# Performance work log

Hardware: AMD Instinct MI355X
Metric: run time of the kernel (lower is better)

The kernel has to match this reference:

```python
import jax, jax.numpy as jnp
import numpy as np

EMBED = 1024
HEADS = 16
HEAD_SIZE = EMBED // HEADS


def setup_inputs() -> dict:
    key = jax.random.key(0)
    kx, kk, kq, kv, kp, kb = jax.random.split(key, 6)
    s = 1.0 / np.sqrt(EMBED)
    return {
        "x": jax.random.normal(kx, (4, 2048, EMBED), dtype=jnp.float32),
        "Wk": jax.random.uniform(kk, (EMBED, EMBED), jnp.float32, -s, s),
        "Wq": jax.random.uniform(kq, (EMBED, EMBED), jnp.float32, -s, s),
        "Wv": jax.random.uniform(kv, (EMBED, EMBED), jnp.float32, -s, s),
        "Wp": jax.random.uniform(kp, (EMBED, EMBED), jnp.float32, -s, s),
        "bp": jax.random.uniform(kb, (EMBED,), jnp.float32, -s, s),
    }


def reference(x, Wk, Wq, Wv, Wp, bp):
    B, T, C = x.shape
    H, D = HEADS, HEAD_SIZE
    # torch nn.Linear: y = x @ W.T
    k = (x @ Wk.T).reshape(B, T, H, D).transpose(0, 2, 1, 3)  # [B,H,T,D]
    q = (x @ Wq.T).reshape(B, T, H, D).transpose(0, 2, 1, 3)
    v = (x @ Wv.T).reshape(B, T, H, D).transpose(0, 2, 1, 3)
    att = jnp.einsum('bhqd,bhkd->bhqk', q, k) * (1.0 / np.sqrt(D))
    causal = jnp.tril(jnp.ones((T, T), dtype=bool))
    att = jnp.where(causal, att, -jnp.inf)
    att = jax.nn.softmax(att, axis=-1)
    # dropout is identity in eval mode
    out = jnp.einsum('bhqk,bhkd->bhqd', att, v)
    out = out.transpose(0, 2, 1, 3).reshape(B, T, C)
    return out @ Wp.T + bp
```

## Files before the change

kernel.cpp:

```cpp
#include <hip/hip_runtime.h>
#include <hip/hip_bf16.h>

typedef __attribute__((ext_vector_type(8))) short bf16x8;
typedef __attribute__((ext_vector_type(4))) float f32x4;

#define DEVINL __device__ __forceinline__

static DEVINL ushort f2b(float f) {
    union { float f; unsigned int u; } v; v.f = f;
    unsigned int u = v.u;
    unsigned int r = (u + 0x7FFFu + ((u >> 16) & 1u)) >> 16;
    return (ushort)r;
}

static DEVINL unsigned int cvtpk(float lo, float hi) {
    unsigned int r;
    asm("v_cvt_pk_bf16_f32 %0, %1, %2" : "=v"(r) : "v"(lo), "v"(hi));
    return r;
}

static DEVINL void gload_lds16(const ushort* g, ushort* l) {
    __builtin_amdgcn_global_load_lds(
        (const __attribute__((address_space(1))) unsigned int*)g,
        (__attribute__((address_space(3))) unsigned int*)l,
        16, 0, 0);
}

static DEVINL int swz(int row, int c) {
    return row * 64 + (((c ^ (row & 7)) & 7) << 3);
}

__global__ void cast_w_kernel(const float* __restrict__ Wq, const float* __restrict__ Wk,
                              const float* __restrict__ Wv, const float* __restrict__ Wp,
                              ushort* __restrict__ out) {
    int idx = blockIdx.x * blockDim.x + threadIdx.x;
    int col4 = idx & 255;
    int row  = idx >> 8;
    int which = row >> 10;
    int r = row & 1023;
    const float* src = (which == 0) ? Wq : (which == 1) ? Wk : (which == 2) ? Wv : Wp;
    float s = (which == 0) ? 0.125f : 1.0f;
    float4 v = ((const float4*)src)[r * 256 + col4];
    ushort4 o;
    o.x = f2b(v.x * s); o.y = f2b(v.y * s); o.z = f2b(v.z * s); o.w = f2b(v.w * s);
    ((ushort4*)out)[idx] = o;
}

__global__ void cast_x_kernel(const float* __restrict__ x, ushort* __restrict__ out) {
    int idx = blockIdx.x * blockDim.x + threadIdx.x;
    float4 v = ((const float4*)x)[idx];
    ushort4 o;
    o.x = f2b(v.x); o.y = f2b(v.y); o.z = f2b(v.z); o.w = f2b(v.w);
    ((ushort4*)out)[idx] = o;
}

template<bool BF16_OUT>
__global__ __launch_bounds__(256) void gemm_bt_kernel(const ushort* __restrict__ A,
                                                      const ushort* __restrict__ B,
                                                      void* __restrict__ Cv,
                                                      const float* __restrict__ bias,
                                                      int M, int N, int K, int gx) {
    __shared__ ushort Al[128 * 64];
    __shared__ ushort Bl[128 * 64];
    const int tid = threadIdx.x;

    const int nwg = (int)gridDim.x;
    const int cpx = nwg >> 3;
    const int orig = (int)blockIdx.x;
    const int wgid = (orig & 7) * cpx + (orig >> 3);
    const int bx = wgid % gx, by = wgid / gx;
    const int m0 = by * 128, n0 = bx * 128;

    const int lane = tid & 63, wid = tid >> 6;
    const int wm = (wid >> 1) * 64, wn = (wid & 1) * 64;
    const int lr = lane & 15, lg = lane >> 4;

    f32x4 acc[4][4];
    #pragma unroll
    for (int i = 0; i < 4; ++i)
        #pragma unroll
        for (int j = 0; j < 4; ++j)
            acc[i][j] = (f32x4){0.f, 0.f, 0.f, 0.f};

    const int grow = wid * 32 + (lane >> 3);
    const int gcol = (((lane & 7) ^ (lane >> 3)) & 7) * 8;
    const ushort* ga = A + (size_t)(m0 + grow) * K + gcol;
    const ushort* gb = B + (size_t)(n0 + grow) * K + gcol;
    ushort* la = &Al[wid * 32 * 64];
    ushort* lb = &Bl[wid * 32 * 64];

    const int nkt = K >> 6;
    for (int kt = 0; kt < nkt; ++kt) {
        const int kof = kt * 64;
        __syncthreads();
        #pragma unroll
        for (int j = 0; j < 4; ++j) {
            gload_lds16(ga + (size_t)(j * 8) * K + kof, la + j * 8 * 64);
            gload_lds16(gb + (size_t)(j * 8) * K + kof, lb + j * 8 * 64);
        }
        __syncthreads();
        #pragma unroll
        for (int kk = 0; kk < 64; kk += 32) {
            bf16x8 af[4], bfr[4];
            #pragma unroll
            for (int mi = 0; mi < 4; ++mi)
                af[mi] = *(const bf16x8*)&Al[swz(wm + mi * 16 + lr, (kk >> 3) + lg)];
            #pragma unroll
            for (int ni = 0; ni < 4; ++ni)
                bfr[ni] = *(const bf16x8*)&Bl[swz(wn + ni * 16 + lr, (kk >> 3) + lg)];
            #pragma unroll
            for (int mi = 0; mi < 4; ++mi)
                #pragma unroll
                for (int ni = 0; ni < 4; ++ni)
                    acc[mi][ni] = __builtin_amdgcn_mfma_f32_16x16x32_bf16(af[mi], bfr[ni], acc[mi][ni], 0, 0, 0);
        }
    }
    #pragma unroll
    for (int mi = 0; mi < 4; ++mi) {
        #pragma unroll
        for (int r = 0; r < 4; ++r) {
            int gm = m0 + wm + mi * 16 + lg * 4 + r;
            #pragma unroll
            for (int ni = 0; ni < 4; ++ni) {
                int gn = n0 + wn + ni * 16 + lr;
                float val = acc[mi][ni][r];
                if (BF16_OUT) {
                    ((ushort*)Cv)[(size_t)gm * N + gn] = f2b(val);
                } else {
                    ((float*)Cv)[(size_t)gm * N + gn] = val + bias[gn];
                }
            }
        }
    }
}

__global__ void transpose_v_kernel(const ushort* __restrict__ QKV, ushort* __restrict__ Vt) {
    __shared__ ushort tile[32][33];
    int t0 = blockIdx.x * 32;
    int n0 = blockIdx.y * 32;
    int tx = threadIdx.x, ty = threadIdx.y;
    #pragma unroll
    for (int i = 0; i < 4; ++i) {
        int row = ty + i * 8;
        tile[row][tx] = QKV[(size_t)(t0 + row) * 3072 + 2048 + n0 + tx];
    }
    __syncthreads();
    #pragma unroll
    for (int i = 0; i < 4; ++i) {
        int row = ty + i * 8;
        Vt[(size_t)(n0 + row) * 8192 + t0 + tx] = tile[tx][row];
    }
}

__global__ __launch_bounds__(256, 3) void attn_kernel(const ushort* __restrict__ QKV,
                                                      const ushort* __restrict__ Vt,
                                                      ushort* __restrict__ O) {
    __shared__ ushort Kl[2][64 * 64];
    __shared__ ushort Vl[2][64 * 64];
    __shared__ ushort Pl[4][32 * 64];

    const int bh = blockIdx.x, b = bh >> 4, h = bh & 15;
    const int qb = (int)gridDim.y - 1 - (int)blockIdx.y;
    const int q0 = qb * 128;
    const int tid = threadIdx.x, lane = tid & 63, w = tid >> 6;
    const int lr = lane & 15, lg = lane >> 4;
    const int qw = q0 + w * 32;

    bf16x8 qf[2][2];
    {
        const ushort* qp = QKV + (size_t)(b * 2048 + qw + lr) * 3072 + h * 64 + lg * 8;
        qf[0][0] = *(const bf16x8*)qp;
        qf[0][1] = *(const bf16x8*)(qp + 32);
        qf[1][0] = *(const bf16x8*)(qp + (size_t)16 * 3072);
        qf[1][1] = *(const bf16x8*)(qp + (size_t)16 * 3072 + 32);
    }

    f32x4 o[4][2];
    #pragma unroll
    for (int di = 0; di < 4; ++di)
        #pragma unroll
        for (int nt_ = 0; nt_ < 2; ++nt_)
            o[di][nt_] = (f32x4){0.f, 0.f, 0.f, 0.f};
    float mrow[2] = {-INFINITY, -INFINITY};
    float lrow[2] = {0.f, 0.f};

    const size_t kbase = (size_t)(b * 2048) * 3072 + 1024 + h * 64;
    const size_t vbase = (size_t)(h * 64) * 8192 + (size_t)b * 2048;
    const int srow = tid >> 2, sc = tid & 3;
    const int ss0 = swz(srow, sc), ss1 = swz(srow, sc + 4);
    char* const pw = (char*)&Pl[w][0];

    const int nt = qb * 2 + 2;
    uint4 kr0, kr1, vr0, vr1;

    #define LOADT(t) do {                                                      \
        const int kv0s = (t) * 64;                                             \
        const ushort* kg = QKV + kbase + (size_t)(kv0s + srow) * 3072;         \
        const ushort* vg = Vt + vbase + (size_t)srow * 8192 + kv0s;            \
        kr0 = *(const uint4*)&kg[sc * 8];                                      \
        kr1 = *(const uint4*)&kg[sc * 8 + 32];                                 \
        vr0 = *(const uint4*)&vg[sc * 8];                                      \
        vr1 = *(const uint4*)&vg[sc * 8 + 32];                                 \
    } while (0)

    #define WRITET(bufi) do {                                                  \
        *(uint4*)&Kl[bufi][ss0] = kr0;                                         \
        *(uint4*)&Kl[bufi][ss1] = kr1;                                         \
        *(uint4*)&Vl[bufi][ss0] = vr0;                                         \
        *(uint4*)&Vl[bufi][ss1] = vr1;                                         \
    } while (0)

    LOADT(0);
    WRITET(0);
    __syncthreads();

    for (int t = 0; t < nt; ++t) {
        const int buf = t & 1;
        const int kv0 = t * 64;
        const bool have_next = (t + 1 < nt);
        if (have_next) LOADT(t + 1);

        if (kv0 <= qw + 31) {
            f32x4 s[4][2];
            #pragma unroll
            for (int mi = 0; mi < 4; ++mi)
                #pragma unroll
                for (int nt_ = 0; nt_ < 2; ++nt_)
                    s[mi][nt_] = (f32x4){0.f, 0.f, 0.f, 0.f};
            __builtin_amdgcn_s_setprio(1);
            #pragma unroll
            for (int ks = 0; ks < 2; ++ks) {
                #pragma unroll
                for (int mi = 0; mi < 4; ++mi) {
                    bf16x8 kf = *(const bf16x8*)&Kl[buf][swz(mi * 16 + lr, ks * 4 + lg)];
                    s[mi][0] = __builtin_amdgcn_mfma_f32_16x16x32_bf16(kf, qf[0][ks], s[mi][0], 0, 0, 0);
                    s[mi][1] = __builtin_amdgcn_mfma_f32_16x16x32_bf16(kf, qf[1][ks], s[mi][1], 0, 0, 0);
                }
            }
            __builtin_amdgcn_s_setprio(0);

            #pragma unroll
            for (int nt_ = 0; nt_ < 2; ++nt_) {
                const int qn = qw + nt_ * 16 + lr;
                const bool full = (kv0 + 63 <= qw + nt_ * 16);
                const int kvb = kv0 + lg * 4;
                float v[4][4];
                #pragma unroll
                for (int mi = 0; mi < 4; ++mi)
                    #pragma unroll
                    for (int r = 0; r < 4; ++r) {
                        float x = s[mi][nt_][r];
                        if (!full) x = (kvb + mi * 16 + r <= qn) ? x : -INFINITY;
                        v[mi][r] = x;
                    }
                float mx0 = fmaxf(fmaxf(v[0][0], v[0][1]), fmaxf(v[0][2], v[0][3]));
                float mx1 = fmaxf(fmaxf(v[1][0], v[1][1]), fmaxf(v[1][2], v[1][3]));
                float mx2 = fmaxf(fmaxf(v[2][0], v[2][1]), fmaxf(v[2][2], v[2][3]));
                float mx3 = fmaxf(fmaxf(v[3][0], v[3][1]), fmaxf(v[3][2], v[3][3]));
                float pmax = fmaxf(fmaxf(mx0, mx1), fmaxf(mx2, mx3));
                pmax = fmaxf(pmax, __shfl_xor(pmax, 16));
                pmax = fmaxf(pmax, __shfl_xor(pmax, 32));

                const bool defer = __all(pmax <= mrow[nt_] + 8.0f);
                float mn;
                if (defer) {
                    mn = mrow[nt_];
                } else {
                    mn = fmaxf(mrow[nt_], pmax);
                    const float al = __expf(mrow[nt_] - mn);
                    lrow[nt_] *= al;
                    #pragma unroll
                    for (int di = 0; di < 4; ++di)
                        #pragma unroll
                        for (int r = 0; r < 4; ++r)
                            o[di][nt_][r] *= al;
                    mrow[nt_] = mn;
                }
                float p[4][4];
                #pragma unroll
                for (int mi = 0; mi < 4; ++mi)
                    #pragma unroll
                    for (int r = 0; r < 4; ++r)
                        p[mi][r] = __expf(v[mi][r] - mn);
                float rs = ((p[0][0] + p[0][1]) + (p[0][2] + p[0][3]))
                         + ((p[1][0] + p[1][1]) + (p[1][2] + p[1][3]))
                         + ((p[2][0] + p[2][1]) + (p[2][2] + p[2][3]))
                         + ((p[3][0] + p[3][1]) + (p[3][2] + p[3][3]));
                rs += __shfl_xor(rs, 16);
                rs += __shfl_xor(rs, 32);
                lrow[nt_] += rs;

                const int rowoff = (nt_ * 16 + lr) * 128;
                const int xr = (lr & 7) << 4;
                #pragma unroll
                for (int mi = 0; mi < 4; ++mi) {
                    uint2 val;
                    val.x = cvtpk(p[mi][0], p[mi][1]);
                    val.y = cvtpk(p[mi][2], p[mi][3]);
                    *(uint2*)(pw + rowoff + ((32 * mi + 8 * lg) ^ xr)) = val;
                }
            }
            asm volatile("s_waitcnt lgkmcnt(0)" ::: "memory");
            __builtin_amdgcn_sched_barrier(0);

            __builtin_amdgcn_s_setprio(1);
            #pragma unroll
            for (int ks = 0; ks < 2; ++ks) {
                bf16x8 pb[2];
                #pragma unroll
                for (int nt_ = 0; nt_ < 2; ++nt_) {
                    const int byteoff = (nt_ * 16 + lr) * 128 + (((64 * ks + 16 * lg)) ^ ((lr & 7) << 4));
                    pb[nt_] = *(const bf16x8*)(pw + byteoff);
                }
                #pragma unroll
                for (int di = 0; di < 4; ++di) {
                    bf16x8 vf = *(const bf16x8*)&Vl[buf][swz(di * 16 + lr, ks * 4 + lg)];
                    o[di][0] = __builtin_amdgcn_mfma_f32_16x16x32_bf16(vf, pb[0], o[di][0], 0, 0, 0);
                    o[di][1] = __builtin_amdgcn_mfma_f32_16x16x32_bf16(vf, pb[1], o[di][1], 0, 0, 0);
                }
            }
            __builtin_amdgcn_s_setprio(0);
        }
        if (have_next) WRITET(buf ^ 1);
        __syncthreads();
    }
    #undef LOADT
    #undef WRITET

    #pragma unroll
    for (int nt_ = 0; nt_ < 2; ++nt_) {
        const float inv = 1.0f / lrow[nt_];
        const int rowoff = (nt_ * 16 + lr) * 128;
        const int xr = (lr & 7) << 4;
        #pragma unroll
        for (int di = 0; di < 4; ++di) {
            uint2 val;
            val.x = cvtpk(o[di][nt_][0] * inv, o[di][nt_][1] * inv);
            val.y = cvtpk(o[di][nt_][2] * inv, o[di][nt_][3] * inv);
            *(uint2*)(pw + rowoff + ((32 * di + 8 * lg) ^ xr)) = val;
        }
    }
    asm volatile("s_waitcnt lgkmcnt(0)" ::: "memory");
    __builtin_amdgcn_sched_barrier(0);
    {
        const int row = lane >> 1;
        const int half = lane & 1;
        const int xr2 = (row & 7) << 4;
        ushort* og = O + (size_t)(b * 2048 + qw + row) * 1024 + h * 64 + half * 32;
        #pragma unroll
        for (int c = 0; c < 4; ++c) {
            uint4 val = *(const uint4*)(pw + row * 128 + ((half * 64 + c * 16) ^ xr2));
            *(uint4*)&og[c * 8] = val;
        }
    }
}

extern "C" void kernel_launch(void* const* d_in, const int* in_sizes, int n_in,
                              void* d_out, int out_size, void* d_ws, size_t ws_size,
                              hipStream_t stream) {
    const float* x  = (const float*)d_in[0];
    const float* Wk = (const float*)d_in[1];
    const float* Wq = (const float*)d_in[2];
    const float* Wv = (const float*)d_in[3];
    const float* Wp = (const float*)d_in[4];
    const float* bp = (const float*)d_in[5];
    float* out = (float*)d_out;

    char* ws = (char*)d_ws;
    ushort* Xb   = (ushort*)(ws);
    ushort* Wcat = (ushort*)(ws + 16777216);
    ushort* QKV  = (ushort*)(ws + 25165824);
    ushort* Vt   = (ushort*)(ws + 75497472);
    ushort* Obuf = (ushort*)(ws + 92274688);

    cast_w_kernel<<<4096, 256, 0, stream>>>(Wq, Wk, Wv, Wp, Wcat);
    cast_x_kernel<<<8192, 256, 0, stream>>>(x, Xb);
    gemm_bt_kernel<true><<<1536, 256, 0, stream>>>(Xb, Wcat, QKV, nullptr, 8192, 3072, 1024, 24);
    transpose_v_kernel<<<dim3(256, 32), dim3(32, 8), 0, stream>>>(QKV, Vt);
    attn_kernel<<<dim3(64, 16), 256, 0, stream>>>(QKV, Vt, Obuf);
    gemm_bt_kernel<false><<<512, 256, 0, stream>>>(Obuf, Wcat + (size_t)3072 * 1024, out, bp, 8192, 1024, 1024, 8);
}
```

Measured before the change: 185.1 us.

## Single-buffer attention K/V LDS, raise occupancy, use exp2 softmax, remap blocks

Folds log2(e) into the Q weight scale so the softmax can use exp2f instead of __expf, and widens the deferred-rescale threshold to match base-2 units. Drops the double-buffered K/V shared tiles to a single buffer with an extra barrier before the write, which cuts LDS per block so launch bounds can request 5 blocks per CU. The grid is flattened to 1D with a custom block-to-(batch, head, q-block) mapping that interleaves heads and keeps heavy causal blocks scheduled first. Risks: the extra sync serializes the LDS write with compute, and the higher occupancy target may force register spills.

```diff
diff --git a/kernel.cpp b/kernel.cpp
--- a/kernel.cpp
+++ b/kernel.cpp
@@ -39,7 +39,7 @@
     int which = row >> 10;
     int r = row & 1023;
     const float* src = (which == 0) ? Wq : (which == 1) ? Wk : (which == 2) ? Wv : Wp;
-    float s = (which == 0) ? 0.125f : 1.0f;
+    float s = (which == 0) ? 0.180336880111f : 1.0f;
     float4 v = ((const float4*)src)[r * 256 + col4];
     ushort4 o;
     o.x = f2b(v.x * s); o.y = f2b(v.y * s); o.z = f2b(v.z * s); o.w = f2b(v.w * s);
@@ -152,15 +152,17 @@
     }
 }
 
-__global__ __launch_bounds__(256, 3) void attn_kernel(const ushort* __restrict__ QKV,
+__global__ __launch_bounds__(256, 5) void attn_kernel(const ushort* __restrict__ QKV,
                                                       const ushort* __restrict__ Vt,
                                                       ushort* __restrict__ O) {
-    __shared__ ushort Kl[2][64 * 64];
-    __shared__ ushort Vl[2][64 * 64];
+    __shared__ ushort Kl[64 * 64];
+    __shared__ ushort Vl[64 * 64];
     __shared__ ushort Pl[4][32 * 64];
 
-    const int bh = blockIdx.x, b = bh >> 4, h = bh & 15;
-    const int qb = (int)gridDim.y - 1 - (int)blockIdx.y;
+    const int flat = (int)blockIdx.x;
+    const int bh = (flat & 7) * 8 + ((flat >> 7) & 7);
+    const int qb = 15 - ((flat >> 3) & 15);
+    const int b = bh >> 4, h = bh & 15;
     const int q0 = qb * 128;
     const int tid = threadIdx.x, lane = tid & 63, w = tid >> 6;
     const int lr = lane & 15, lg = lane >> 4;
@@ -203,19 +205,18 @@
         vr1 = *(const uint4*)&vg[sc * 8 + 32];                                 \
     } while (0)
 
-    #define WRITET(bufi) do {                                                  \
-        *(uint4*)&Kl[bufi][ss0] = kr0;                                         \
-        *(uint4*)&Kl[bufi][ss1] = kr1;                                         \
-        *(uint4*)&Vl[bufi][ss0] = vr0;                                         \
-        *(uint4*)&Vl[bufi][ss1] = vr1;                                         \
+    #define WRITET() do {                                                      \
+        *(uint4*)&Kl[ss0] = kr0;                                               \
+        *(uint4*)&Kl[ss1] = kr1;                                               \
+        *(uint4*)&Vl[ss0] = vr0;                                               \
+        *(uint4*)&Vl[ss1] = vr1;                                               \
     } while (0)
 
     LOADT(0);
-    WRITET(0);
+    WRITET();
     __syncthreads();
 
     for (int t = 0; t < nt; ++t) {
-        const int buf = t & 1;
         const int kv0 = t * 64;
         const bool have_next = (t + 1 < nt);
         if (have_next) LOADT(t + 1);
@@ -232,7 +233,7 @@
             for (int ks = 0; ks < 2; ++ks) {
                 #pragma unroll
                 for (int mi = 0; mi < 4; ++mi) {
-                    bf16x8 kf = *(const bf16x8*)&Kl[buf][swz(mi * 16 + lr, ks * 4 + lg)];
+                    bf16x8 kf = *(const bf16x8*)&Kl[swz(mi * 16 + lr, ks * 4 + lg)];
                     s[mi][0] = __builtin_amdgcn_mfma_f32_16x16x32_bf16(kf, qf[0][ks], s[mi][0], 0, 0, 0);
                     s[mi][1] = __builtin_amdgcn_mfma_f32_16x16x32_bf16(kf, qf[1][ks], s[mi][1], 0, 0, 0);
                 }
@@ -261,13 +262,13 @@
                 pmax = fmaxf(pmax, __shfl_xor(pmax, 16));
                 pmax = fmaxf(pmax, __shfl_xor(pmax, 32));
 
-                const bool defer = __all(pmax <= mrow[nt_] + 8.0f);
+                const bool defer = __all(pmax <= mrow[nt_] + 11.5f);
                 float mn;
                 if (defer) {
                     mn = mrow[nt_];
                 } else {
                     mn = fmaxf(mrow[nt_], pmax);
-                    const float al = __expf(mrow[nt_] - mn);
+                    const float al = exp2f(mrow[nt_] - mn);
                     lrow[nt_] *= al;
                     #pragma unroll
                     for (int di = 0; di < 4; ++di)
@@ -281,7 +282,7 @@
                 for (int mi = 0; mi < 4; ++mi)
                     #pragma unroll
                     for (int r = 0; r < 4; ++r)
-                        p[mi][r] = __expf(v[mi][r] - mn);
+                        p[mi][r] = exp2f(v[mi][r] - mn);
                 float rs = ((p[0][0] + p[0][1]) + (p[0][2] + p[0][3]))
                          + ((p[1][0] + p[1][1]) + (p[1][2] + p[1][3]))
                          + ((p[2][0] + p[2][1]) + (p[2][2] + p[2][3]))
@@ -314,14 +315,15 @@
                 }
                 #pragma unroll
                 for (int di = 0; di < 4; ++di) {
-                    bf16x8 vf = *(const bf16x8*)&Vl[buf][swz(di * 16 + lr, ks * 4 + lg)];
+                    bf16x8 vf = *(const bf16x8*)&Vl[swz(di * 16 + lr, ks * 4 + lg)];
                     o[di][0] = __builtin_amdgcn_mfma_f32_16x16x32_bf16(vf, pb[0], o[di][0], 0, 0, 0);
                     o[di][1] = __builtin_amdgcn_mfma_f32_16x16x32_bf16(vf, pb[1], o[di][1], 0, 0, 0);
                 }
             }
             __builtin_amdgcn_s_setprio(0);
         }
-        if (have_next) WRITET(buf ^ 1);
+        __syncthreads();
+        if (have_next) WRITET();
         __syncthreads();
     }
     #undef LOADT
@@ -377,6 +379,6 @@
     cast_x_kernel<<<8192, 256, 0, stream>>>(x, Xb);
     gemm_bt_kernel<true><<<1536, 256, 0, stream>>>(Xb, Wcat, QKV, nullptr, 8192, 3072, 1024, 24);
     transpose_v_kernel<<<dim3(256, 32), dim3(32, 8), 0, stream>>>(QKV, Vt);
-    attn_kernel<<<dim3(64, 16), 256, 0, stream>>>(QKV, Vt, Obuf);
+    attn_kernel<<<1024, 256, 0, stream>>>(QKV, Vt, Obuf);
     gemm_bt_kernel<false><<<512, 256, 0, stream>>>(Obuf, Wcat + (size_t)3072 * 1024, out, bp, 8192, 1024, 1024, 8);
 }
```

New measurement: 484.1 us. 162% more time.

## Fold log2e into Q scale, use exp2, and halve per-wave P staging LDS

Applied to the files above, without the earlier changes.

The Q weight scale now folds in log2(e), so the softmax uses exp2f directly instead of __expf. This removes a multiply per exponential, and the lazy-rescale threshold is converted to log2 units to match. The per-wave P staging buffer is halved: P is written and read back one k-slice at a time, and the output epilogue is done in two 16-row halves. This cuts LDS use per block, which may allow higher occupancy, at the cost of extra LDS waits and sched barriers inside the PV loop.

```diff
diff --git a/kernel.cpp b/kernel.cpp
--- a/kernel.cpp
+++ b/kernel.cpp
@@ -39,7 +39,7 @@
     int which = row >> 10;
     int r = row & 1023;
     const float* src = (which == 0) ? Wq : (which == 1) ? Wk : (which == 2) ? Wv : Wp;
-    float s = (which == 0) ? 0.125f : 1.0f;
+    float s = (which == 0) ? 0.180336880111f : 1.0f;
     float4 v = ((const float4*)src)[r * 256 + col4];
     ushort4 o;
     o.x = f2b(v.x * s); o.y = f2b(v.y * s); o.z = f2b(v.z * s); o.w = f2b(v.w * s);
@@ -157,7 +157,7 @@
                                                       ushort* __restrict__ O) {
     __shared__ ushort Kl[2][64 * 64];
     __shared__ ushort Vl[2][64 * 64];
-    __shared__ ushort Pl[4][32 * 64];
+    __shared__ ushort Pl[4][32 * 32];
 
     const int bh = blockIdx.x, b = bh >> 4, h = bh & 15;
     const int qb = (int)gridDim.y - 1 - (int)blockIdx.y;
@@ -189,6 +189,7 @@
     const int srow = tid >> 2, sc = tid & 3;
     const int ss0 = swz(srow, sc), ss1 = swz(srow, sc + 4);
     char* const pw = (char*)&Pl[w][0];
+    const int psx = ((lr >> 1) & 3) << 4;
 
     const int nt = qb * 2 + 2;
     uint4 kr0, kr1, vr0, vr1;
@@ -239,6 +240,7 @@
             }
             __builtin_amdgcn_s_setprio(0);
 
+            unsigned int px[2][4], py[2][4];
             #pragma unroll
             for (int nt_ = 0; nt_ < 2; ++nt_) {
                 const int qn = qw + nt_ * 16 + lr;
@@ -261,13 +263,13 @@
                 pmax = fmaxf(pmax, __shfl_xor(pmax, 16));
                 pmax = fmaxf(pmax, __shfl_xor(pmax, 32));
 
-                const bool defer = __all(pmax <= mrow[nt_] + 8.0f);
+                const bool defer = __all(pmax <= mrow[nt_] + 11.5f);
                 float mn;
                 if (defer) {
                     mn = mrow[nt_];
                 } else {
                     mn = fmaxf(mrow[nt_], pmax);
-                    const float al = __expf(mrow[nt_] - mn);
+                    const float al = exp2f(mrow[nt_] - mn);
                     lrow[nt_] *= al;
                     #pragma unroll
                     for (int di = 0; di < 4; ++di)
@@ -281,7 +283,7 @@
                 for (int mi = 0; mi < 4; ++mi)
                     #pragma unroll
                     for (int r = 0; r < 4; ++r)
-                        p[mi][r] = __expf(v[mi][r] - mn);
+                        p[mi][r] = exp2f(v[mi][r] - mn);
                 float rs = ((p[0][0] + p[0][1]) + (p[0][2] + p[0][3]))
                          + ((p[1][0] + p[1][1]) + (p[1][2] + p[1][3]))
                          + ((p[2][0] + p[2][1]) + (p[2][2] + p[2][3]))
@@ -290,36 +292,42 @@
                 rs += __shfl_xor(rs, 32);
                 lrow[nt_] += rs;
 
-                const int rowoff = (nt_ * 16 + lr) * 128;
-                const int xr = (lr & 7) << 4;
                 #pragma unroll
                 for (int mi = 0; mi < 4; ++mi) {
-                    uint2 val;
-                    val.x = cvtpk(p[mi][0], p[mi][1]);
-                    val.y = cvtpk(p[mi][2], p[mi][3]);
-                    *(uint2*)(pw + rowoff + ((32 * mi + 8 * lg) ^ xr)) = val;
+                    px[nt_][mi] = cvtpk(p[mi][0], p[mi][1]);
+                    py[nt_][mi] = cvtpk(p[mi][2], p[mi][3]);
                 }
             }
-            asm volatile("s_waitcnt lgkmcnt(0)" ::: "memory");
-            __builtin_amdgcn_sched_barrier(0);
-
-            __builtin_amdgcn_s_setprio(1);
+
             #pragma unroll
             for (int ks = 0; ks < 2; ++ks) {
+                #pragma unroll
+                for (int nt_ = 0; nt_ < 2; ++nt_) {
+                    const int rb = (nt_ * 16 + lr) * 64;
+                    #pragma unroll
+                    for (int m1 = 0; m1 < 2; ++m1) {
+                        const int mi = 2 * ks + m1;
+                        uint2 val;
+                        val.x = px[nt_][mi];
+                        val.y = py[nt_][mi];
+                        *(uint2*)(pw + rb + ((m1 * 32 + lg * 8) ^ psx)) = val;
+                    }
+                }
+                asm volatile("s_waitcnt lgkmcnt(0)" ::: "memory");
+                __builtin_amdgcn_sched_barrier(0);
+                __builtin_amdgcn_s_setprio(1);
                 bf16x8 pb[2];
                 #pragma unroll
-                for (int nt_ = 0; nt_ < 2; ++nt_) {
-                    const int byteoff = (nt_ * 16 + lr) * 128 + (((64 * ks + 16 * lg)) ^ ((lr & 7) << 4));
-                    pb[nt_] = *(const bf16x8*)(pw + byteoff);
-                }
+                for (int nt_ = 0; nt_ < 2; ++nt_)
+                    pb[nt_] = *(const bf16x8*)(pw + (nt_ * 16 + lr) * 64 + ((lg * 16) ^ psx));
                 #pragma unroll
                 for (int di = 0; di < 4; ++di) {
                     bf16x8 vf = *(const bf16x8*)&Vl[buf][swz(di * 16 + lr, ks * 4 + lg)];
                     o[di][0] = __builtin_amdgcn_mfma_f32_16x16x32_bf16(vf, pb[0], o[di][0], 0, 0, 0);
                     o[di][1] = __builtin_amdgcn_mfma_f32_16x16x32_bf16(vf, pb[1], o[di][1], 0, 0, 0);
                 }
+                __builtin_amdgcn_s_setprio(0);
             }
-            __builtin_amdgcn_s_setprio(0);
         }
         if (have_next) WRITET(buf ^ 1);
         __syncthreads();
@@ -330,27 +338,22 @@
     #pragma unroll
     for (int nt_ = 0; nt_ < 2; ++nt_) {
         const float inv = 1.0f / lrow[nt_];
-        const int rowoff = (nt_ * 16 + lr) * 128;
-        const int xr = (lr & 7) << 4;
         #pragma unroll
         for (int di = 0; di < 4; ++di) {
             uint2 val;
             val.x = cvtpk(o[di][nt_][0] * inv, o[di][nt_][1] * inv);
             val.y = cvtpk(o[di][nt_][2] * inv, o[di][nt_][3] * inv);
-            *(uint2*)(pw + rowoff + ((32 * di + 8 * lg) ^ xr)) = val;
-        }
-    }
-    asm volatile("s_waitcnt lgkmcnt(0)" ::: "memory");
-    __builtin_amdgcn_sched_barrier(0);
-    {
-        const int row = lane >> 1;
-        const int half = lane & 1;
-        const int xr2 = (row & 7) << 4;
-        ushort* og = O + (size_t)(b * 2048 + qw + row) * 1024 + h * 64 + half * 32;
-        #pragma unroll
-        for (int c = 0; c < 4; ++c) {
-            uint4 val = *(const uint4*)(pw + row * 128 + ((half * 64 + c * 16) ^ xr2));
-            *(uint4*)&og[c * 8] = val;
+            *(uint2*)(pw + lr * 128 + di * 32 + lg * 8) = val;
+        }
+        asm volatile("s_waitcnt lgkmcnt(0)" ::: "memory");
+        __builtin_amdgcn_sched_barrier(0);
+        {
+            const int row = lane >> 2, c = lane & 3;
+            ushort* og = O + (size_t)(b * 2048 + qw + nt_ * 16 + row) * 1024 + h * 64 + c * 16;
+            uint4 v0 = *(const uint4*)(pw + row * 128 + c * 32);
+            uint4 v1 = *(const uint4*)(pw + row * 128 + c * 32 + 16);
+            *(uint4*)og = v0;
+            *(uint4*)(og + 8) = v1;
         }
     }
 }
```

Result: slower. 196.3 us (+6.0%).

## Feed softmax probabilities to PV MFMA from registers, use exp2 with folded scale

Applied to the files above, without the earlier changes.

The probability tile no longer round-trips through a per-wave LDS buffer. P values stay in registers as packed bf16 and feed 16x16x16 MFMAs directly, with the V fragment loads reshaped to match that register layout. This removes LDS stores, the wait and the reloads, and frees the Pl shared array, which could raise occupancy; the epilogue reuses Kl as scratch. The Q scale now folds in log2(e) so exp2f replaces __expf, and the deferred-rescale threshold is raised to match base 2. The trade is twice as many, smaller MFMA instructions for the PV product.

```diff
diff --git a/kernel.cpp b/kernel.cpp
--- a/kernel.cpp
+++ b/kernel.cpp
@@ -2,6 +2,7 @@
 #include <hip/hip_bf16.h>
 
 typedef __attribute__((ext_vector_type(8))) short bf16x8;
+typedef __attribute__((ext_vector_type(4))) short bf16x4;
 typedef __attribute__((ext_vector_type(4))) float f32x4;
 
 #define DEVINL __device__ __forceinline__
@@ -39,7 +40,7 @@
     int which = row >> 10;
     int r = row & 1023;
     const float* src = (which == 0) ? Wq : (which == 1) ? Wk : (which == 2) ? Wv : Wp;
-    float s = (which == 0) ? 0.125f : 1.0f;
+    float s = (which == 0) ? 0.180336880111f : 1.0f;
     float4 v = ((const float4*)src)[r * 256 + col4];
     ushort4 o;
     o.x = f2b(v.x * s); o.y = f2b(v.y * s); o.z = f2b(v.z * s); o.w = f2b(v.w * s);
@@ -157,7 +158,6 @@
                                                       ushort* __restrict__ O) {
     __shared__ ushort Kl[2][64 * 64];
     __shared__ ushort Vl[2][64 * 64];
-    __shared__ ushort Pl[4][32 * 64];
 
     const int bh = blockIdx.x, b = bh >> 4, h = bh & 15;
     const int qb = (int)gridDim.y - 1 - (int)blockIdx.y;
@@ -188,7 +188,6 @@
     const size_t vbase = (size_t)(h * 64) * 8192 + (size_t)b * 2048;
     const int srow = tid >> 2, sc = tid & 3;
     const int ss0 = swz(srow, sc), ss1 = swz(srow, sc + 4);
-    char* const pw = (char*)&Pl[w][0];
 
     const int nt = qb * 2 + 2;
     uint4 kr0, kr1, vr0, vr1;
@@ -239,6 +238,7 @@
             }
             __builtin_amdgcn_s_setprio(0);
 
+            unsigned int px[2][4], py[2][4];
             #pragma unroll
             for (int nt_ = 0; nt_ < 2; ++nt_) {
                 const int qn = qw + nt_ * 16 + lr;
@@ -261,13 +261,13 @@
                 pmax = fmaxf(pmax, __shfl_xor(pmax, 16));
                 pmax = fmaxf(pmax, __shfl_xor(pmax, 32));
 
-                const bool defer = __all(pmax <= mrow[nt_] + 8.0f);
+                const bool defer = __all(pmax <= mrow[nt_] + 11.5f);
                 float mn;
                 if (defer) {
                     mn = mrow[nt_];
                 } else {
                     mn = fmaxf(mrow[nt_], pmax);
-                    const float al = __expf(mrow[nt_] - mn);
+                    const float al = exp2f(mrow[nt_] - mn);
                     lrow[nt_] *= al;
                     #pragma unroll
                     for (int di = 0; di < 4; ++di)
@@ -281,7 +281,7 @@
                 for (int mi = 0; mi < 4; ++mi)
                     #pragma unroll
                     for (int r = 0; r < 4; ++r)
-                        p[mi][r] = __expf(v[mi][r] - mn);
+                        p[mi][r] = exp2f(v[mi][r] - mn);
                 float rs = ((p[0][0] + p[0][1]) + (p[0][2] + p[0][3]))
                          + ((p[1][0] + p[1][1]) + (p[1][2] + p[1][3]))
                          + ((p[2][0] + p[2][1]) + (p[2][2] + p[2][3]))
@@ -290,33 +290,27 @@
                 rs += __shfl_xor(rs, 32);
                 lrow[nt_] += rs;
 
-                const int rowoff = (nt_ * 16 + lr) * 128;
-                const int xr = (lr & 7) << 4;
                 #pragma unroll
                 for (int mi = 0; mi < 4; ++mi) {
-                    uint2 val;
-                    val.x = cvtpk(p[mi][0], p[mi][1]);
-                    val.y = cvtpk(p[mi][2], p[mi][3]);
-                    *(uint2*)(pw + rowoff + ((32 * mi + 8 * lg) ^ xr)) = val;
+                    px[nt_][mi] = cvtpk(p[mi][0], p[mi][1]);
+                    py[nt_][mi] = cvtpk(p[mi][2], p[mi][3]);
                 }
             }
-            asm volatile("s_waitcnt lgkmcnt(0)" ::: "memory");
-            __builtin_amdgcn_sched_barrier(0);
 
             __builtin_amdgcn_s_setprio(1);
             #pragma unroll
-            for (int ks = 0; ks < 2; ++ks) {
-                bf16x8 pb[2];
+            for (int mi = 0; mi < 4; ++mi) {
+                bf16x4 pb[2];
                 #pragma unroll
                 for (int nt_ = 0; nt_ < 2; ++nt_) {
-                    const int byteoff = (nt_ * 16 + lr) * 128 + (((64 * ks + 16 * lg)) ^ ((lr & 7) << 4));
-                    pb[nt_] = *(const bf16x8*)(pw + byteoff);
+                    uint2 tmp; tmp.x = px[nt_][mi]; tmp.y = py[nt_][mi];
+                    pb[nt_] = *(const bf16x4*)&tmp;
                 }
                 #pragma unroll
                 for (int di = 0; di < 4; ++di) {
-                    bf16x8 vf = *(const bf16x8*)&Vl[buf][swz(di * 16 + lr, ks * 4 + lg)];
-                    o[di][0] = __builtin_amdgcn_mfma_f32_16x16x32_bf16(vf, pb[0], o[di][0], 0, 0, 0);
-                    o[di][1] = __builtin_amdgcn_mfma_f32_16x16x32_bf16(vf, pb[1], o[di][1], 0, 0, 0);
+                    bf16x4 vf = *(const bf16x4*)&Vl[buf][swz(di * 16 + lr, 2 * mi + (lg >> 1)) + (lg & 1) * 4];
+                    o[di][0] = __builtin_amdgcn_mfma_f32_16x16x16bf16_1k(vf, pb[0], o[di][0], 0, 0, 0);
+                    o[di][1] = __builtin_amdgcn_mfma_f32_16x16x16bf16_1k(vf, pb[1], o[di][1], 0, 0, 0);
                 }
             }
             __builtin_amdgcn_s_setprio(0);
@@ -327,6 +321,7 @@
     #undef LOADT
     #undef WRITET
 
+    char* const pw = (char*)&Kl[0][0] + w * 4096;
     #pragma unroll
     for (int nt_ = 0; nt_ < 2; ++nt_) {
         const float inv = 1.0f / lrow[nt_];
```

Measured after the change: 199.1 us. 7.5% more time.
